# Kernel optimization log

Measured on AMD Instinct MI355X. Metric: run time of the kernel, lower is better.

Reference implementation:

```python
import jax, jax.numpy as jnp
import numpy as np

B, ENC_LEN, DEC_LEN = 4, 1024, 256
ENC_H, DEC_H, ATTN = 1024, 1024, 256


def setup_inputs() -> dict:
    key = jax.random.key(0)
    k1, k2, k3, k4, k5, k6 = jax.random.split(key, 6)
    scale = 0.02
    return {
        "encoded_seq": jax.random.normal(k1, (B, ENC_LEN, ENC_H), jnp.float32),
        "decoder_state": jax.random.normal(k2, (B, DEC_LEN, DEC_H), jnp.float32),
        "input_pad_mask": jnp.ones((B, ENC_LEN), jnp.float32),
        "Wh": jax.random.normal(k3, (ENC_H, ATTN), jnp.float32) * scale,
        "Ws": jax.random.normal(k4, (DEC_H, ATTN), jnp.float32) * scale,
        "bs": jax.random.normal(k5, (ATTN,), jnp.float32) * scale,
        "v": jax.random.normal(k6, (ATTN,), jnp.float32) * scale,
    }


def reference(encoded_seq, decoder_state, input_pad_mask, Wh, Ws, bs, v):
    # projections: [B, dec, A] and [B, enc, A]
    proj_dec = jnp.einsum('bdh,ha->bda', decoder_state, Ws) + bs
    proj_enc = jnp.einsum('beh,ha->bea', encoded_seq, Wh)
    # additive score: tanh(broadcast add) then dot with selector vector v
    added = jnp.tanh(proj_dec[:, :, None, :] + proj_enc[:, None, :, :])  # [B,dec,enc,A]
    attn_logits = jnp.einsum('bdea,a->bde', added, v)                    # [B,dec,enc]
    attn_weights = jax.nn.softmax(attn_logits, axis=-1)
    attn_weights2 = attn_weights * input_pad_mask[:, None, :]
    attn_renorm = attn_weights2 / jnp.sum(attn_weights2, axis=-1, keepdims=True)
    context = jnp.einsum('bde,beh->bdh', attn_renorm, encoded_seq)       # [B,dec,enc_h]
    return context, attn_renorm
```

## Files before the change

kernel.cpp:

```cpp
#include <hip/hip_runtime.h>
#include <hip/hip_bf16.h>

#define BB 4
#define ENC_LEN 1024
#define DEC_LEN 256
#define ENC_H 1024
#define ATTN_A 256

#define C2F 2.8853900817779268f

typedef short bf16x8 __attribute__((ext_vector_type(8)));
typedef float f32x4 __attribute__((ext_vector_type(4)));
typedef float f32x2 __attribute__((ext_vector_type(2)));
typedef unsigned int u32x2 __attribute__((ext_vector_type(2)));

union BF8 {
  uint4 q;
  bf16x8 v;
};

static __device__ __forceinline__ unsigned short f2bf(float x) {
  union {
    float f;
    unsigned int u;
  } c;
  c.f = x;
  unsigned int r = c.u + 0x7FFFu + ((c.u >> 16) & 1u);
  return (unsigned short)(r >> 16);
}

__global__ __launch_bounds__(256) void prep_k(
    const float* __restrict__ Wh, const float* __restrict__ Ws,
    const float* __restrict__ enc, const float* __restrict__ dec,
    unsigned short* __restrict__ WhT, unsigned short* __restrict__ WsT,
    unsigned short* __restrict__ encT, unsigned short* __restrict__ encB,
    unsigned short* __restrict__ decB) {
  __shared__ unsigned short T[64][68];
  const int wb = blockIdx.x;
  const int t = threadIdx.x;
  const int lr = t >> 4;
  const int lc4 = (t & 15) * 4;

  if (wb >= 1152) {
    const int q = wb - 1152;
    const int r0 = (q >> 4) * 64;
    const int c0 = (q & 15) * 64;
#pragma unroll
    for (int p = 0; p < 4; ++p) {
      const int r = lr + p * 16;
      const float4 v = *(const float4*)&dec[(long)(r0 + r) * ENC_H + c0 + lc4];
      ushort4 o;
      o.x = f2bf(v.x);
      o.y = f2bf(v.y);
      o.z = f2bf(v.z);
      o.w = f2bf(v.w);
      *(ushort4*)&decB[(long)(r0 + r) * ENC_H + c0 + lc4] = o;
    }
    return;
  }

  const float* in;
  unsigned short* out;
  unsigned short* out2 = nullptr;
  int R, C, bx, by;
  if (wb < 128) {
    in = (wb < 64) ? Wh : Ws;
    out = (wb < 64) ? WhT : WsT;
    const int tt = wb & 63;
    R = ENC_H;
    C = ATTN_A;
    bx = tt & 3;
    by = tt >> 2;
  } else {
    const int tt0 = wb - 128;
    const int b = tt0 >> 8;
    const int tt = tt0 & 255;
    in = enc + (long)b * ENC_LEN * ENC_H;
    out = encT + (long)b * ENC_H * ENC_LEN;
    out2 = encB + (long)b * ENC_LEN * ENC_H;
    R = ENC_LEN;
    C = ENC_H;
    bx = tt & 15;
    by = tt >> 4;
  }
  const int r0 = by * 64;
  const int c0 = bx * 64;

#pragma unroll
  for (int p = 0; p < 4; ++p) {
    const int r = lr + p * 16;
    const float4 v = *(const float4*)&in[(long)(r0 + r) * C + c0 + lc4];
    ushort4 o;
    o.x = f2bf(v.x);
    o.y = f2bf(v.y);
    o.z = f2bf(v.z);
    o.w = f2bf(v.w);
    *(ushort4*)&T[r][lc4] = o;
    if (out2) *(ushort4*)&out2[(long)(r0 + r) * C + c0 + lc4] = o;
  }
  __syncthreads();
#pragma unroll
  for (int p = 0; p < 4; ++p) {
    const int c = lr + p * 16;
    ushort4 o;
    o.x = T[lc4 + 0][c];
    o.y = T[lc4 + 1][c];
    o.z = T[lc4 + 2][c];
    o.w = T[lc4 + 3][c];
    *(ushort4*)&out[(long)(c0 + c) * R + r0 + lc4] = o;
  }
}

__global__ __launch_bounds__(256) void pgemm(const unsigned short* __restrict__ decB,
                                             const unsigned short* __restrict__ encB,
                                             const unsigned short* __restrict__ WsT,
                                             const unsigned short* __restrict__ WhT,
                                             const float* __restrict__ bs,
                                             float* __restrict__ Ed,
                                             float* __restrict__ Ee) {
  __shared__ unsigned short As[64][72];
  __shared__ unsigned short Bs[64][72];

  const int bid = blockIdx.x;
  const bool isPD = bid < 64;
  const unsigned short* A;
  const unsigned short* BT;
  float* out;
  int ldc, m0, n0;
  if (isPD) {
    A = decB;
    BT = WsT;
    out = Ed;
    ldc = ATTN_A;
    m0 = (bid >> 2) * 64;
    n0 = (bid & 3) * 64;
  } else {
    const int q = bid - 64;
    const int b = q >> 6;
    const int r = q & 63;
    A = WhT;
    BT = encB + (long)b * ENC_LEN * ENC_H;
    out = Ee + (long)b * ATTN_A * ENC_LEN;
    ldc = ENC_LEN;
    m0 = (r >> 4) * 64;
    n0 = (r & 15) * 64;
  }

  const int tid = threadIdx.x;
  const int lane = tid & 63;
  const int wave = tid >> 6;
  const int quad = lane >> 4;
  const int l16 = lane & 15;
  const int wm = (wave >> 1) * 32;
  const int wn = (wave & 1) * 32;
  const int sr = tid >> 2;
  const int sk = (tid & 3) * 16;

  f32x4 acc[2][2] = {{{0.f, 0.f, 0.f, 0.f}, {0.f, 0.f, 0.f, 0.f}},
                     {{0.f, 0.f, 0.f, 0.f}, {0.f, 0.f, 0.f, 0.f}}};

  const unsigned short* Ap = A + (long)(m0 + sr) * ENC_H + sk;
  const unsigned short* Bp = BT + (long)(n0 + sr) * ENC_H + sk;

  uint4 a0 = *(const uint4*)(Ap);
  uint4 a1 = *(const uint4*)(Ap + 8);
  uint4 b0 = *(const uint4*)(Bp);
  uint4 b1 = *(const uint4*)(Bp + 8);

  for (int k0 = 0; k0 < 1024; k0 += 64) {
    __syncthreads();
    *(uint4*)&As[sr][sk] = a0;
    *(uint4*)&As[sr][sk + 8] = a1;
    *(uint4*)&Bs[sr][sk] = b0;
    *(uint4*)&Bs[sr][sk + 8] = b1;
    const int kn = (k0 + 64 < 1024) ? (k0 + 64) : 0;
    a0 = *(const uint4*)(Ap + kn);
    a1 = *(const uint4*)(Ap + kn + 8);
    b0 = *(const uint4*)(Bp + kn);
    b1 = *(const uint4*)(Bp + kn + 8);
    __syncthreads();

#pragma unroll
    for (int h = 0; h < 2; ++h) {
      bf16x8 af[2], bfr[2];
#pragma unroll
      for (int i = 0; i < 2; ++i) {
        BF8 t;
        t.q = *(const uint4*)&As[wm + i * 16 + l16][h * 32 + quad * 8];
        af[i] = t.v;
      }
#pragma unroll
      for (int j = 0; j < 2; ++j) {
        BF8 t;
        t.q = *(const uint4*)&Bs[wn + j * 16 + l16][h * 32 + quad * 8];
        bfr[j] = t.v;
      }
#pragma unroll
      for (int i = 0; i < 2; ++i)
#pragma unroll
        for (int j = 0; j < 2; ++j)
          acc[i][j] = __builtin_amdgcn_mfma_f32_16x16x32_bf16(af[i], bfr[j],
                                                              acc[i][j], 0, 0, 0);
    }
  }

#pragma unroll
  for (int j = 0; j < 2; ++j) {
    const int col = n0 + wn + j * 16 + l16;
    const float cb = isPD ? (C2F * bs[col]) : 0.f;
#pragma unroll
    for (int i = 0; i < 2; ++i) {
      const int row = m0 + wm + i * 16 + quad * 4;
#pragma unroll
      for (int r = 0; r < 4; ++r)
        out[(long)(row + r) * ldc + col] =
            __builtin_amdgcn_exp2f(C2F * acc[i][j][r] + cb);
    }
  }
}

__global__ __launch_bounds__(256) void logits_k(const float* __restrict__ Ee,
                                                const float* __restrict__ Ed,
                                                const float* __restrict__ v,
                                                float* __restrict__ p0) {
  const int tid = threadIdx.x;
  const int e = blockIdx.x * 256 + tid;
  const int d0 = blockIdx.y * 8;
  const int b = blockIdx.z;

  __shared__ float Eds[256][8];
  __shared__ float vv[256];

#pragma unroll
  for (int dd = 0; dd < 8; ++dd)
    Eds[tid][dd] = Ed[(long)(b * DEC_LEN + d0 + dd) * ATTN_A + tid];
  vv[tid] = -2.0f * v[tid];
  __syncthreads();

  f32x2 acc2[4] = {{0.f, 0.f}, {0.f, 0.f}, {0.f, 0.f}, {0.f, 0.f}};
  const float* pe = Ee + (long)b * (ATTN_A * ENC_LEN) + e;

  float pn[8];
#pragma unroll
  for (int u = 0; u < 8; ++u) pn[u] = pe[(long)u * ENC_LEN];

  for (int a8 = 0; a8 < 256; a8 += 8) {
    float ee[8];
#pragma unroll
    for (int u = 0; u < 8; ++u) ee[u] = pn[u];
    const int an = (a8 + 8 < 256) ? (a8 + 8) : 0;
#pragma unroll
    for (int u = 0; u < 8; ++u) pn[u] = pe[(long)(an + u) * ENC_LEN];

    const float4 vL = *(const float4*)&vv[a8];
    const float4 vH = *(const float4*)&vv[a8 + 4];
    const float vs[8] = {vL.x, vL.y, vL.z, vL.w, vH.x, vH.y, vH.z, vH.w};

#pragma unroll
    for (int ddp = 0; ddp < 4; ++ddp) {
      f32x2 dn[8];
#pragma unroll
      for (int u = 0; u < 8; ++u) {
        const f32x2 ed2 = *(const f32x2*)&Eds[a8 + u][ddp * 2];
        dn[u] = ed2 * ee[u] + 1.0f;
      }
      const f32x2 pA = dn[0] * dn[1];
      const f32x2 pB = dn[2] * dn[3];
      const f32x2 pC = dn[4] * dn[5];
      const f32x2 pD = dn[6] * dn[7];
      const f32x2 sA = dn[1] * vs[0] + dn[0] * vs[1];
      const f32x2 sB = dn[3] * vs[2] + dn[2] * vs[3];
      const f32x2 sC = dn[5] * vs[4] + dn[4] * vs[5];
      const f32x2 sD = dn[7] * vs[6] + dn[6] * vs[7];
      const f32x2 P1 = pA * pB;
      const f32x2 P2 = pC * pD;
      const f32x2 S1 = sA * pB + sB * pA;
      const f32x2 S2 = sC * pD + sD * pC;
      const f32x2 num = S1 * P2 + S2 * P1;
      const f32x2 D = P1 * P2;
      f32x2 r;
      r.x = __builtin_amdgcn_rcpf(D.x);
      r.y = __builtin_amdgcn_rcpf(D.y);
      acc2[ddp] += num * r;
    }
  }

  const long base = ((long)(b * DEC_LEN + d0) * ENC_LEN) + e;
#pragma unroll
  for (int ddp = 0; ddp < 4; ++ddp) {
    p0[base + (long)(2 * ddp) * ENC_LEN] = acc2[ddp].x;
    p0[base + (long)(2 * ddp + 1) * ENC_LEN] = acc2[ddp].y;
  }
}

__global__ __launch_bounds__(256) void softmax2_k(float* __restrict__ p0,
                                                  const float* __restrict__ mask,
                                                  unsigned short* __restrict__ attnB) {
  const int row = blockIdx.x;
  const int b = row >> 8;
  const int tid = threadIdx.x;
  float* rp = p0 + (long)row * ENC_LEN;
  const float* mp = mask + b * ENC_LEN;
  unsigned short* rb = attnB + (long)row * ENC_LEN;

  float l[4], m[4];
#pragma unroll
  for (int j = 0; j < 4; ++j) {
    l[j] = rp[tid + 256 * j];
    m[j] = mp[tid + 256 * j];
  }

  __shared__ float redmax[4];
  __shared__ float redsum[4];
  const int lane = tid & 63;
  const int wid = tid >> 6;

  float tm = fmaxf(fmaxf(l[0], l[1]), fmaxf(l[2], l[3]));
#pragma unroll
  for (int off = 1; off < 64; off <<= 1) tm = fmaxf(tm, __shfl_xor(tm, off, 64));
  if (lane == 0) redmax[wid] = tm;
  __syncthreads();
  const float rmax = fmaxf(fmaxf(redmax[0], redmax[1]), fmaxf(redmax[2], redmax[3]));

  const float LOG2E = 1.4426950408889634f;
  float p[4];
  float ts = 0.f;
#pragma unroll
  for (int j = 0; j < 4; ++j) {
    p[j] = __builtin_amdgcn_exp2f((l[j] - rmax) * LOG2E) * m[j];
    ts += p[j];
  }
#pragma unroll
  for (int off = 1; off < 64; off <<= 1) ts += __shfl_xor(ts, off, 64);
  if (lane == 0) redsum[wid] = ts;
  __syncthreads();
  const float rsum = redsum[0] + redsum[1] + redsum[2] + redsum[3];

  const float inv = 1.0f / rsum;
#pragma unroll
  for (int j = 0; j < 4; ++j) {
    const float w = p[j] * inv;
    rp[tid + 256 * j] = w;
    rb[tid + 256 * j] = f2bf(w);
  }
}

__global__ __launch_bounds__(256) void cgemm(const unsigned short* __restrict__ attnB,
                                             const unsigned short* __restrict__ encT,
                                             float* __restrict__ ctx) {
  __shared__ unsigned short As[64][72];
  __shared__ unsigned short Bs[64][72];

  const int b = blockIdx.z;
  const unsigned short* A = attnB + (long)b * DEC_LEN * ENC_LEN;
  const unsigned short* BT = encT + (long)b * ENC_H * ENC_LEN;
  float* C = ctx + (long)b * DEC_LEN * ENC_H;

  const int tid = threadIdx.x;
  const int lane = tid & 63;
  const int wave = tid >> 6;
  const int quad = lane >> 4;
  const int l16 = lane & 15;
  const int wm = (wave >> 1) * 32;
  const int wn = (wave & 1) * 32;
  const int m0 = blockIdx.y * 64;
  const int n0 = blockIdx.x * 64;
  const int sr = tid >> 2;
  const int sk = (tid & 3) * 16;

  f32x4 acc[2][2] = {{{0.f, 0.f, 0.f, 0.f}, {0.f, 0.f, 0.f, 0.f}},
                     {{0.f, 0.f, 0.f, 0.f}, {0.f, 0.f, 0.f, 0.f}}};

  const unsigned short* Ap = A + (long)(m0 + sr) * ENC_LEN + sk;
  const unsigned short* Bp = BT + (long)(n0 + sr) * ENC_LEN + sk;

  uint4 a0 = *(const uint4*)(Ap);
  uint4 a1 = *(const uint4*)(Ap + 8);
  uint4 b0 = *(const uint4*)(Bp);
  uint4 b1 = *(const uint4*)(Bp + 8);

  for (int k0 = 0; k0 < 1024; k0 += 64) {
    __syncthreads();
    *(uint4*)&As[sr][sk] = a0;
    *(uint4*)&As[sr][sk + 8] = a1;
    *(uint4*)&Bs[sr][sk] = b0;
    *(uint4*)&Bs[sr][sk + 8] = b1;
    const int kn = (k0 + 64 < 1024) ? (k0 + 64) : 0;
    a0 = *(const uint4*)(Ap + kn);
    a1 = *(const uint4*)(Ap + kn + 8);
    b0 = *(const uint4*)(Bp + kn);
    b1 = *(const uint4*)(Bp + kn + 8);
    __syncthreads();

#pragma unroll
    for (int h = 0; h < 2; ++h) {
      bf16x8 af[2], bfr[2];
#pragma unroll
      for (int i = 0; i < 2; ++i) {
        BF8 t;
        t.q = *(const uint4*)&As[wm + i * 16 + l16][h * 32 + quad * 8];
        af[i] = t.v;
      }
#pragma unroll
      for (int j = 0; j < 2; ++j) {
        BF8 t;
        t.q = *(const uint4*)&Bs[wn + j * 16 + l16][h * 32 + quad * 8];
        bfr[j] = t.v;
      }
#pragma unroll
      for (int i = 0; i < 2; ++i)
#pragma unroll
        for (int j = 0; j < 2; ++j)
          acc[i][j] = __builtin_amdgcn_mfma_f32_16x16x32_bf16(af[i], bfr[j],
                                                              acc[i][j], 0, 0, 0);
    }
  }

#pragma unroll
  for (int j = 0; j < 2; ++j) {
    const int col = n0 + wn + j * 16 + l16;
#pragma unroll
    for (int i = 0; i < 2; ++i) {
      const int row = m0 + wm + i * 16 + quad * 4;
#pragma unroll
      for (int r = 0; r < 4; ++r) C[(long)(row + r) * ENC_H + col] = acc[i][j][r];
    }
  }
}

template <int OMODE, bool BIAS>
__global__ __launch_bounds__(256) void gemm64(const float* __restrict__ A,
                                              const float* __restrict__ B,
                                              const float* __restrict__ bias,
                                              float* __restrict__ C,
                                              int K, int lda, int ldb, int ldc,
                                              long sA, long sB, long sC) {
  const int bz = blockIdx.z;
  A += (long)bz * sA;
  B += (long)bz * sB;
  C += (long)bz * sC;

  const int tid = threadIdx.x;
  const int tx = tid & 15;
  const int ty = tid >> 4;

  __shared__ float As2[16][64];
  __shared__ float Bs2[16][64];

  float acc[4][4];
#pragma unroll
  for (int i = 0; i < 4; ++i)
#pragma unroll
    for (int j = 0; j < 4; ++j) acc[i][j] = 0.f;

  const int ar = tid >> 2;
  const int ak4 = (tid & 3) << 2;
  const int br = tid >> 4;
  const int bn4 = (tid & 15) << 2;

  const float* Aload = A + (long)(blockIdx.y * 64 + ar) * lda + ak4;
  const float* Bload = B + (long)br * ldb + blockIdx.x * 64 + bn4;

  for (int k0 = 0; k0 < K; k0 += 16) {
    const float4 av = *(const float4*)(Aload + k0);
    const float4 bv = *(const float4*)(Bload + (long)k0 * ldb);
    __syncthreads();
    As2[ak4 + 0][ar] = av.x;
    As2[ak4 + 1][ar] = av.y;
    As2[ak4 + 2][ar] = av.z;
    As2[ak4 + 3][ar] = av.w;
    *(float4*)&Bs2[br][bn4] = bv;
    __syncthreads();
#pragma unroll
    for (int kk = 0; kk < 16; ++kk) {
      const float4 a4 = *(const float4*)&As2[kk][ty << 2];
      const float4 b4 = *(const float4*)&Bs2[kk][tx << 2];
      const float am[4] = {a4.x, a4.y, a4.z, a4.w};
      const float bn[4] = {b4.x, b4.y, b4.z, b4.w};
#pragma unroll
      for (int i = 0; i < 4; ++i)
#pragma unroll
        for (int j = 0; j < 4; ++j) acc[i][j] = fmaf(am[i], bn[j], acc[i][j]);
    }
  }

  if (OMODE == 0) {
    const int row0 = blockIdx.y * 64 + (ty << 2);
    const int col0 = blockIdx.x * 64 + (tx << 2);
    float4 bb4 = make_float4(0.f, 0.f, 0.f, 0.f);
    if (BIAS) bb4 = *(const float4*)&bias[col0];
#pragma unroll
    for (int i = 0; i < 4; ++i) {
      float4 o;
      o.x = acc[i][0] + bb4.x;
      o.y = acc[i][1] + bb4.y;
      o.z = acc[i][2] + bb4.z;
      o.w = acc[i][3] + bb4.w;
      *(float4*)&C[(long)(row0 + i) * ldc + col0] = o;
    }
  } else {
#pragma unroll
    for (int i = 0; i < 4; ++i) {
      const int gr = blockIdx.y * 64 + (ty << 2) + i;
      const int b = gr >> 10;
      const int e = gr & 1023;
#pragma unroll
      for (int j = 0; j < 4; ++j) {
        const int col = blockIdx.x * 64 + (tx << 2) + j;
        C[(long)b * (ATTN_A * ENC_LEN) + (long)col * ENC_LEN + e] = acc[i][j];
      }
    }
  }
}

__global__ __launch_bounds__(256) void logits_fb(const float* __restrict__ peT,
                                                 const float* __restrict__ pd,
                                                 const float* __restrict__ v,
                                                 float* __restrict__ out) {
  const int tid = threadIdx.x;
  const int e = blockIdx.x * 256 + tid;
  const int d0 = blockIdx.y * 8;
  const int b = blockIdx.z;

  __shared__ float cpd[ATTN_A][8];
  __shared__ float vv[ATTN_A];

  {
    const int a = tid;
#pragma unroll
    for (int dd = 0; dd < 8; ++dd)
      cpd[a][dd] = C2F * pd[((b * DEC_LEN + d0 + dd) * ATTN_A) + a];
    vv[a] = -2.0f * v[a];
  }
  __syncthreads();

  float acc[8] = {0.f, 0.f, 0.f, 0.f, 0.f, 0.f, 0.f, 0.f};
  const float* pe = peT + (long)b * (ATTN_A * ENC_LEN) + e;

  for (int a = 0; a < ATTN_A; a += 4) {
    float pes[4];
#pragma unroll
    for (int u = 0; u < 4; ++u) pes[u] = pe[(long)(a + u) * ENC_LEN];
#pragma unroll
    for (int u = 0; u < 4; ++u) {
      const float cpe = C2F * pes[u];
      const float vu = vv[a + u];
      const float4 c0 = *(const float4*)&cpd[a + u][0];
      const float4 c1 = *(const float4*)&cpd[a + u][4];
      const float cd[8] = {c0.x, c0.y, c0.z, c0.w, c1.x, c1.y, c1.z, c1.w};
#pragma unroll
      for (int dd = 0; dd < 8; ++dd) {
        const float x = cd[dd] + cpe;
        const float ex = __builtin_amdgcn_exp2f(x);
        const float r = __builtin_amdgcn_rcpf(ex + 1.0f);
        acc[dd] = fmaf(vu, r, acc[dd]);
      }
    }
  }

  const long base = ((long)(b * DEC_LEN + d0) * ENC_LEN) + e;
#pragma unroll
  for (int dd = 0; dd < 8; ++dd) out[base + (long)dd * ENC_LEN] = acc[dd];
}

__global__ __launch_bounds__(256) void softmax_fb(float* __restrict__ attn,
                                                  const float* __restrict__ mask) {
  const int row = blockIdx.x;
  const int b = row >> 8;
  const int tid = threadIdx.x;
  float* rp = attn + (long)row * ENC_LEN;
  const float* mp = mask + b * ENC_LEN;

  float l[4], m[4];
#pragma unroll
  for (int j = 0; j < 4; ++j) {
    l[j] = rp[tid + 256 * j];
    m[j] = mp[tid + 256 * j];
  }

  __shared__ float redmax[4];
  __shared__ float redsum[4];
  const int lane = tid & 63;
  const int wid = tid >> 6;

  float tm = fmaxf(fmaxf(l[0], l[1]), fmaxf(l[2], l[3]));
#pragma unroll
  for (int off = 1; off < 64; off <<= 1) tm = fmaxf(tm, __shfl_xor(tm, off, 64));
  if (lane == 0) redmax[wid] = tm;
  __syncthreads();
  const float rmax = fmaxf(fmaxf(redmax[0], redmax[1]), fmaxf(redmax[2], redmax[3]));

  const float LOG2E = 1.4426950408889634f;
  float p[4];
  float ts = 0.f;
#pragma unroll
  for (int j = 0; j < 4; ++j) {
    p[j] = __builtin_amdgcn_exp2f((l[j] - rmax) * LOG2E) * m[j];
    ts += p[j];
  }
#pragma unroll
  for (int off = 1; off < 64; off <<= 1) ts += __shfl_xor(ts, off, 64);
  if (lane == 0) redsum[wid] = ts;
  __syncthreads();
  const float rsum = redsum[0] + redsum[1] + redsum[2] + redsum[3];

  const float inv = 1.0f / rsum;
#pragma unroll
  for (int j = 0; j < 4; ++j) rp[tid + 256 * j] = p[j] * inv;
}

extern "C" void kernel_launch(void* const* d_in, const int* in_sizes, int n_in,
                              void* d_out, int out_size, void* d_ws, size_t ws_size,
                              hipStream_t stream) {
  const float* enc = (const float*)d_in[0];
  const float* dec = (const float*)d_in[1];
  const float* mask = (const float*)d_in[2];
  const float* Wh = (const float*)d_in[3];
  const float* Ws = (const float*)d_in[4];
  const float* bs = (const float*)d_in[5];
  const float* v = (const float*)d_in[6];

  float* ctx = (float*)d_out;
  float* attn = ctx + (long)BB * DEC_LEN * ENC_H;

  const long N_ED = 1024L * ATTN_A;
  const long N_EE = (long)BB * ATTN_A * ENC_LEN;
  const long N_ENC = (long)BB * ENC_H * ENC_LEN;
  const long N_W = (long)ATTN_A * ENC_H;
  const long N_DEC = 1024L * ENC_H;
  const long N_ATT = (long)BB * DEC_LEN * ENC_LEN;
  const size_t FAST_WS =
      (N_ED + N_EE) * 4 + (N_ENC + 2 * N_W + N_ENC + N_DEC + N_ATT) * 2;

  if (ws_size >= FAST_WS) {
    float* Ed = (float*)d_ws;
    float* Ee = Ed + N_ED;
    unsigned short* encT = (unsigned short*)(Ee + N_EE);
    unsigned short* WhT = encT + N_ENC;
    unsigned short* WsT = WhT + N_W;
    unsigned short* encB = WsT + N_W;
    unsigned short* decB = encB + N_ENC;
    unsigned short* attnB = decB + N_DEC;

    prep_k<<<dim3(1408, 1, 1), 256, 0, stream>>>(Wh, Ws, enc, dec, WhT, WsT, encT,
                                                 encB, decB);
    pgemm<<<dim3(320, 1, 1), 256, 0, stream>>>(decB, encB, WsT, WhT, bs, Ed, Ee);
    logits_k<<<dim3(4, 32, BB), 256, 0, stream>>>(Ee, Ed, v, attn);
    softmax2_k<<<dim3(BB * DEC_LEN, 1, 1), 256, 0, stream>>>(attn, mask, attnB);
    cgemm<<<dim3(16, 4, BB), 256, 0, stream>>>(attnB, encT, ctx);
  } else {
    float* pd = (float*)d_ws;
    float* peT = pd + (long)BB * DEC_LEN * ATTN_A;

    gemm64<0, true><<<dim3(ATTN_A / 64, (BB * DEC_LEN) / 64, 1), 256, 0, stream>>>(
        dec, Ws, bs, pd, ENC_H, ENC_H, ATTN_A, ATTN_A, 0, 0, 0);
    gemm64<1, false><<<dim3(ATTN_A / 64, (BB * ENC_LEN) / 64, 1), 256, 0, stream>>>(
        enc, Wh, nullptr, peT, ENC_H, ENC_H, ATTN_A, 0, 0, 0, 0);
    logits_fb<<<dim3(ENC_LEN / 256, DEC_LEN / 8, BB), 256, 0, stream>>>(peT, pd, v,
                                                                        attn);
    softmax_fb<<<dim3(BB * DEC_LEN, 1, 1), 256, 0, stream>>>(attn, mask);
    gemm64<0, false><<<dim3(ENC_H / 64, DEC_LEN / 64, BB), 256, 0, stream>>>(
        attn, enc, nullptr, ctx, ENC_LEN, ENC_LEN, ENC_H, ENC_H,
        (long)DEC_LEN * ENC_LEN, (long)ENC_LEN * ENC_H, (long)DEC_LEN * ENC_H);
  }
}
```

Before: 131.4 us.

## Move encoder transpose into logits kernel and drop softmax max pass

```diff
diff --git a/kernel.cpp b/kernel.cpp
--- a/kernel.cpp
+++ b/kernel.cpp
@@ -33,70 +33,58 @@
     const float* __restrict__ Wh, const float* __restrict__ Ws,
     const float* __restrict__ enc, const float* __restrict__ dec,
     unsigned short* __restrict__ WhT, unsigned short* __restrict__ WsT,
-    unsigned short* __restrict__ encT, unsigned short* __restrict__ encB,
-    unsigned short* __restrict__ decB) {
+    unsigned short* __restrict__ encB, unsigned short* __restrict__ decB) {
   __shared__ unsigned short T[64][68];
   const int wb = blockIdx.x;
   const int t = threadIdx.x;
-  const int lr = t >> 4;
-  const int lc4 = (t & 15) * 4;
-
-  if (wb >= 1152) {
-    const int q = wb - 1152;
-    const int r0 = (q >> 4) * 64;
-    const int c0 = (q & 15) * 64;
-#pragma unroll
-    for (int p = 0; p < 4; ++p) {
-      const int r = lr + p * 16;
-      const float4 v = *(const float4*)&dec[(long)(r0 + r) * ENC_H + c0 + lc4];
+
+  if (wb >= 128) {
+    const float* in;
+    unsigned short* out;
+    long base;
+    if (wb < 1152) {
+      in = enc;
+      out = encB;
+      base = (long)(wb - 128) * 4096;
+    } else {
+      in = dec;
+      out = decB;
+      base = (long)(wb - 1152) * 4096;
+    }
+#pragma unroll
+    for (int k = 0; k < 4; ++k) {
+      const long i = base + (long)(t + k * 256) * 4;
+      const float4 v = *(const float4*)&in[i];
       ushort4 o;
       o.x = f2bf(v.x);
       o.y = f2bf(v.y);
       o.z = f2bf(v.z);
       o.w = f2bf(v.w);
-      *(ushort4*)&decB[(long)(r0 + r) * ENC_H + c0 + lc4] = o;
+      *(ushort4*)&out[i] = o;
     }
     return;
   }
 
-  const float* in;
-  unsigned short* out;
-  unsigned short* out2 = nullptr;
-  int R, C, bx, by;
-  if (wb < 128) {
-    in = (wb < 64) ? Wh : Ws;
-    out = (wb < 64) ? WhT : WsT;
-    const int tt = wb & 63;
-    R = ENC_H;
-    C = ATTN_A;
-    bx = tt & 3;
-    by = tt >> 2;
-  } else {
-    const int tt0 = wb - 128;
-    const int b = tt0 >> 8;
-    const int tt = tt0 & 255;
-    in = enc + (long)b * ENC_LEN * ENC_H;
-    out = encT + (long)b * ENC_H * ENC_LEN;
-    out2 = encB + (long)b * ENC_LEN * ENC_H;
-    R = ENC_LEN;
-    C = ENC_H;
-    bx = tt & 15;
-    by = tt >> 4;
-  }
+  const int lr = t >> 4;
+  const int lc4 = (t & 15) * 4;
+  const float* in = (wb < 64) ? Wh : Ws;
+  unsigned short* out = (wb < 64) ? WhT : WsT;
+  const int tt = wb & 63;
+  const int bx = tt & 3;
+  const int by = tt >> 2;
   const int r0 = by * 64;
   const int c0 = bx * 64;
 
 #pragma unroll
   for (int p = 0; p < 4; ++p) {
     const int r = lr + p * 16;
-    const float4 v = *(const float4*)&in[(long)(r0 + r) * C + c0 + lc4];
+    const float4 v = *(const float4*)&in[(long)(r0 + r) * ATTN_A + c0 + lc4];
     ushort4 o;
     o.x = f2bf(v.x);
     o.y = f2bf(v.y);
     o.z = f2bf(v.z);
     o.w = f2bf(v.w);
     *(ushort4*)&T[r][lc4] = o;
-    if (out2) *(ushort4*)&out2[(long)(r0 + r) * C + c0 + lc4] = o;
   }
   __syncthreads();
 #pragma unroll
@@ -107,7 +95,7 @@
     o.y = T[lc4 + 1][c];
     o.z = T[lc4 + 2][c];
     o.w = T[lc4 + 3][c];
-    *(ushort4*)&out[(long)(c0 + c) * R + r0 + lc4] = o;
+    *(ushort4*)&out[(long)(c0 + c) * ENC_H + r0 + lc4] = o;
   }
 }
 
@@ -219,17 +207,58 @@
   }
 }
 
-__global__ __launch_bounds__(256) void logits_k(const float* __restrict__ Ee,
-                                                const float* __restrict__ Ed,
-                                                const float* __restrict__ v,
-                                                float* __restrict__ p0) {
+__global__ __launch_bounds__(256) void logits_enc_k(
+    const float* __restrict__ Ee, const float* __restrict__ Ed,
+    const float* __restrict__ v, float* __restrict__ p0,
+    const float* __restrict__ enc, unsigned short* __restrict__ encT) {
+  const int bid = blockIdx.x;
   const int tid = threadIdx.x;
-  const int e = blockIdx.x * 256 + tid;
-  const int d0 = blockIdx.y * 8;
-  const int b = blockIdx.z;
-
+
+  __shared__ unsigned short T[64][68];
   __shared__ float Eds[256][8];
   __shared__ float vv[256];
+
+  if (bid < 1024) {
+    const int b = bid >> 8;
+    const int tt = bid & 255;
+    const float* in = enc + (long)b * ENC_LEN * ENC_H;
+    unsigned short* out = encT + (long)b * ENC_H * ENC_LEN;
+    const int bx = tt & 15;
+    const int by = tt >> 4;
+    const int r0 = by * 64;
+    const int c0 = bx * 64;
+    const int lr = tid >> 4;
+    const int lc4 = (tid & 15) * 4;
+
+#pragma unroll
+    for (int p = 0; p < 4; ++p) {
+      const int r = lr + p * 16;
+      const float4 w = *(const float4*)&in[(long)(r0 + r) * ENC_H + c0 + lc4];
+      ushort4 o;
+      o.x = f2bf(w.x);
+      o.y = f2bf(w.y);
+      o.z = f2bf(w.z);
+      o.w = f2bf(w.w);
+      *(ushort4*)&T[r][lc4] = o;
+    }
+    __syncthreads();
+#pragma unroll
+    for (int p = 0; p < 4; ++p) {
+      const int c = lr + p * 16;
+      ushort4 o;
+      o.x = T[lc4 + 0][c];
+      o.y = T[lc4 + 1][c];
+      o.z = T[lc4 + 2][c];
+      o.w = T[lc4 + 3][c];
+      *(ushort4*)&out[(long)(c0 + c) * ENC_LEN + r0 + lc4] = o;
+    }
+    return;
+  }
+
+  const int lb = bid - 1024;
+  const int e = (lb & 3) * 256 + tid;
+  const int d0 = ((lb >> 2) & 31) * 8;
+  const int b = lb >> 7;
 
 #pragma unroll
   for (int dd = 0; dd < 8; ++dd)
@@ -310,24 +339,16 @@
     m[j] = mp[tid + 256 * j];
   }
 
-  __shared__ float redmax[4];
   __shared__ float redsum[4];
   const int lane = tid & 63;
   const int wid = tid >> 6;
 
-  float tm = fmaxf(fmaxf(l[0], l[1]), fmaxf(l[2], l[3]));
-#pragma unroll
-  for (int off = 1; off < 64; off <<= 1) tm = fmaxf(tm, __shfl_xor(tm, off, 64));
-  if (lane == 0) redmax[wid] = tm;
-  __syncthreads();
-  const float rmax = fmaxf(fmaxf(redmax[0], redmax[1]), fmaxf(redmax[2], redmax[3]));
-
   const float LOG2E = 1.4426950408889634f;
   float p[4];
   float ts = 0.f;
 #pragma unroll
   for (int j = 0; j < 4; ++j) {
-    p[j] = __builtin_amdgcn_exp2f((l[j] - rmax) * LOG2E) * m[j];
+    p[j] = __builtin_amdgcn_exp2f(l[j] * LOG2E) * m[j];
     ts += p[j];
   }
 #pragma unroll
@@ -642,10 +663,10 @@
     unsigned short* decB = encB + N_ENC;
     unsigned short* attnB = decB + N_DEC;
 
-    prep_k<<<dim3(1408, 1, 1), 256, 0, stream>>>(Wh, Ws, enc, dec, WhT, WsT, encT,
-                                                 encB, decB);
+    prep_k<<<dim3(1408, 1, 1), 256, 0, stream>>>(Wh, Ws, enc, dec, WhT, WsT, encB,
+                                                 decB);
     pgemm<<<dim3(320, 1, 1), 256, 0, stream>>>(decB, encB, WsT, WhT, bs, Ed, Ee);
-    logits_k<<<dim3(4, 32, BB), 256, 0, stream>>>(Ee, Ed, v, attn);
+    logits_enc_k<<<dim3(1536, 1, 1), 256, 0, stream>>>(Ee, Ed, v, attn, enc, encT);
     softmax2_k<<<dim3(BB * DEC_LEN, 1, 1), 256, 0, stream>>>(attn, mask, attnB);
     cgemm<<<dim3(16, 4, BB), 256, 0, stream>>>(attnB, encT, ctx);
   } else {
```

Result: slower. 137.4 us (+4.6%).
